# Optimization experiments

Measured on AMD Instinct MI355X. Metric: run time of the kernel, lower is better.

The kernel has to match this reference:

```python
import jax, jax.numpy as jnp
import numpy as np

N, S, E, H = 2, 2048, 1024, 16
D = E // H  # head dim = 64


def setup_inputs() -> dict:
    key = jax.random.key(0)
    ks = jax.random.split(key, 9)
    queries = jax.random.normal(ks[0], (N, S, E), dtype=jnp.float32)
    keys = jax.random.normal(ks[1], (N, S, E), dtype=jnp.float32)
    values = jax.random.normal(ks[2], (N, S, E), dtype=jnp.float32)
    mask = jax.random.randint(ks[3], (N, H, S, S), 0, 2, dtype=jnp.int32)
    # torch nn.Linear weights: shape (out_features, in_features), y = x @ W.T
    sc = 1.0 / np.sqrt(E)
    Wq = jax.random.uniform(ks[4], (E, E), jnp.float32, -sc, sc)
    Wk = jax.random.uniform(ks[5], (E, E), jnp.float32, -sc, sc)
    Wv = jax.random.uniform(ks[6], (E, E), jnp.float32, -sc, sc)
    Wo = jax.random.uniform(ks[7], (E, E), jnp.float32, -sc, sc)
    bo = jax.random.uniform(ks[8], (E,), jnp.float32, -sc, sc)
    return {"queries": queries, "keys": keys, "values": values, "mask": mask,
            "Wq": Wq, "Wk": Wk, "Wv": Wv, "Wo": Wo, "bo": bo}


def reference(queries, keys, values, mask, Wq, Wk, Wv, Wo, bo):
    n, d_q, _ = queries.shape
    d_k = keys.shape[1]
    q = (queries @ Wq.T).reshape(n, d_q, H, D)
    k = (keys @ Wk.T).reshape(n, d_k, H, D)
    v = (values @ Wv.T).reshape(n, d_k, H, D)
    energy = jnp.einsum('nqhd,nkhd->nhqk', q, k)
    energy = jnp.where(mask == 0, jnp.float32(-1e20), energy)
    # NOTE: module scales by sqrt of KEY SEQUENCE LENGTH, not head dim
    attn = jax.nn.softmax(energy / (d_k ** 0.5), axis=3)
    out = jnp.einsum('nhql,nlhd->nqhd', attn, v).reshape(n, d_q, E)
    return out @ Wo.T + bo
```

## Files before the change

kernel.cpp:

```cpp
#include <hip/hip_runtime.h>
#include <hip/hip_bf16.h>

#define DEVI __device__ __forceinline__

typedef __bf16 bf16x8 __attribute__((ext_vector_type(8)));
typedef float f32x4 __attribute__((ext_vector_type(4)));
typedef unsigned short u16x4 __attribute__((ext_vector_type(4)));
typedef unsigned int u32x2 __attribute__((ext_vector_type(2)));
typedef unsigned long long ull;
typedef ull u64x2 __attribute__((ext_vector_type(2)));

constexpr int Nn = 2, Ss = 2048, Ee = 1024, Hh = 16;
constexpr int Ms = Nn * Ss;
constexpr float SCALE = 0.022097086912079608f;
constexpr int NCH = 524288;

constexpr size_t SZ_X   = (size_t)Ms * Ee;
constexpr size_t EEc    = (size_t)Ee * Ee;
constexpr size_t OFF_QB = 0;
constexpr size_t OFF_KB = SZ_X;
constexpr size_t OFF_VB = 2 * SZ_X;
constexpr size_t OFF_XQ = 3 * SZ_X;
constexpr size_t OFF_W  = 6 * SZ_X;
constexpr size_t OFF_PACK = 6 * SZ_X + 4 * EEc;
constexpr size_t OFF_ATTN = OFF_XQ;

DEVI unsigned short f2bf(float f) {
  unsigned int u = __builtin_bit_cast(unsigned int, f);
  u += 0x7fffu + ((u >> 16) & 1u);
  return (unsigned short)(u >> 16);
}

DEVI void async16(const void* g, void* l) {
  __builtin_amdgcn_global_load_lds(
      (const __attribute__((address_space(1))) void*)g,
      (__attribute__((address_space(3))) void*)l, 16, 0, 0);
}

DEVI f32x4 mfma_bf16(bf16x8 a, bf16x8 b, f32x4 c) {
  return __builtin_amdgcn_mfma_f32_16x16x32_bf16(a, b, c, 0, 0, 0);
}

DEVI unsigned cvt_pk_bf16(float lo, float hi) {
  unsigned r;
  asm("v_cvt_pk_bf16_f32 %0, %1, %2" : "=v"(r) : "v"(lo), "v"(hi));
  return r;
}

__global__ __launch_bounds__(256) void cvt_batch(
    const float* __restrict__ s0, const float* __restrict__ s1,
    const float* __restrict__ s2, const float* __restrict__ s3,
    unsigned short* __restrict__ dbase, size_t dstride, int n4)
{
  const float* s = (blockIdx.z == 0) ? s0 : (blockIdx.z == 1) ? s1
                 : (blockIdx.z == 2) ? s2 : s3;
  unsigned short* d = dbase + (size_t)blockIdx.z * dstride;
  const int i = blockIdx.x * 256 + threadIdx.x;
  if (i >= n4) return;
  const float4 v = reinterpret_cast<const float4*>(s)[i];
  u16x4 o = { f2bf(v.x), f2bf(v.y), f2bf(v.z), f2bf(v.w) };
  reinterpret_cast<u16x4*>(d)[i] = o;
}

__global__ __launch_bounds__(256) void qkv_pack(
    const unsigned short* __restrict__ Xq,
    const unsigned short* __restrict__ W,
    unsigned short* __restrict__ QKout,
    unsigned short* __restrict__ Vtout,
    const int* __restrict__ mask,
    ull* __restrict__ P64)
{
  constexpr int K = 1024;
  __shared__ unsigned short As[128 * 32];
  __shared__ unsigned short Bs[128 * 32];
  const int b = blockIdx.x;

  const unsigned short *A, *B;
  unsigned short* C;
  int ldC, m0, n0;
  if (b < 512) {
    const int z = b >> 8, by = (b >> 3) & 31, bx = b & 7;
    A = Xq + (size_t)z * SZ_X;  B = W + (size_t)z * EEc;
    C = QKout + (size_t)z * SZ_X;  ldC = Ee;  m0 = by * 128;  n0 = bx * 128;
  } else {
    const int v = b - 512, bx = v & 31, by = v >> 5;
    A = W + 2 * EEc;  B = Xq + 2 * SZ_X;
    C = Vtout;  ldC = Ms;  m0 = by * 128;  n0 = bx * 128;
  }

  const int tid = threadIdx.x;
  const int lane = tid & 63, w = tid >> 6;
  const int lr = lane & 15, lg = lane >> 4;
  const int wr = (w >> 1) * 64, wc = (w & 1) * 64;

  const f32x4 zero = {0.f, 0.f, 0.f, 0.f};
  f32x4 acc[4][4];
  for (int a = 0; a < 4; ++a)
    for (int c = 0; c < 4; ++c) acc[a][c] = zero;

  const int cblock = b * 768;

  for (int s = 0; s < 32; ++s) {
    const int k0 = s * 32;
#pragma unroll
    for (int ii = 0; ii < 2; ++ii) {
      const int i = 2 * w + ii;
      const int boff = i * 1024 + lane * 16;
      const int row = boff >> 6;
      const int colb = boff & 63;
      const char* ga = (const char*)A + ((size_t)(m0 + row) * K + k0) * 2 + colb;
      const char* gb = (const char*)B + ((size_t)(n0 + row) * K + k0) * 2 + colb;
      async16(ga, (char*)As + i * 1024);
      async16(gb, (char*)Bs + i * 1024);
    }

    const int cbase = cblock + s * 24 + w * 6;
    int pm[6][4];
#pragma unroll
    for (int i = 0; i < 6; ++i) {
      const int ch = cbase + i;
      if (ch < NCH) {
        const int* mp = mask + (size_t)ch * 256 + lane;
        pm[i][0] = __builtin_nontemporal_load(mp);
        pm[i][1] = __builtin_nontemporal_load(mp + 64);
        pm[i][2] = __builtin_nontemporal_load(mp + 128);
        pm[i][3] = __builtin_nontemporal_load(mp + 192);
      }
    }

    __syncthreads();

    bf16x8 aF[4], bF[4];
#pragma unroll
    for (int rb = 0; rb < 4; ++rb)
      aF[rb] = *(const bf16x8*)(As + (wr + rb * 16 + lr) * 32 + lg * 8);
#pragma unroll
    for (int cb = 0; cb < 4; ++cb)
      bF[cb] = *(const bf16x8*)(Bs + (wc + cb * 16 + lr) * 32 + lg * 8);
#pragma unroll
    for (int rb = 0; rb < 4; ++rb)
#pragma unroll
      for (int cb = 0; cb < 4; ++cb)
        acc[rb][cb] = mfma_bf16(aF[rb], bF[cb], acc[rb][cb]);

#pragma unroll
    for (int i = 0; i < 6; ++i) {
      const int ch = cbase + i;
      if (ch < NCH) {
        const ull b0 = __ballot(pm[i][0] != 0);
        const ull b1 = __ballot(pm[i][1] != 0);
        const ull b2 = __ballot(pm[i][2] != 0);
        const ull b3 = __ballot(pm[i][3] != 0);
        if (lane < 2) {
          u64x2 v;
          v[0] = lane == 0 ? b0 : b2;
          v[1] = lane == 0 ? b1 : b3;
          *(u64x2*)(P64 + (size_t)ch * 4 + lane * 2) = v;
        }
      }
    }

    __syncthreads();
  }

#pragma unroll
  for (int rb = 0; rb < 4; ++rb)
#pragma unroll
    for (int cb = 0; cb < 4; ++cb)
#pragma unroll
      for (int j = 0; j < 4; ++j) {
        const int row = m0 + wr + rb * 16 + lg * 4 + j;
        const int col = n0 + wc + cb * 16 + lr;
        C[(size_t)row * ldC + col] = f2bf(acc[rb][cb][j]);
      }
}

__global__ __launch_bounds__(256) void attn_kernel(
    const unsigned short* __restrict__ Qb,
    const unsigned short* __restrict__ Kb,
    const unsigned short* __restrict__ Vtb,
    const ull* __restrict__ P64,
    unsigned short* __restrict__ Ob)
{
  __shared__ unsigned short Kl0[64 * 64], Kl1[64 * 64];
  __shared__ unsigned short Vl0[64 * 64], Vl1[64 * 64];
  __shared__ unsigned short Pw[4 * 32 * 72];

  const int tid = threadIdx.x;
  const int lane = tid & 63, w = tid >> 6;
  const int lr = lane & 15, lg = lane >> 4;

  const int lid = blockIdx.x;
  const int xcd = lid & 7, slot = lid >> 3;
  const int g = xcd + 8 * (slot >> 4);
  const int n = g >> 4, h = g & 15;
  const int q0 = (slot & 15) * 128;

  bf16x8 aQ[2][2];
#pragma unroll
  for (int qb = 0; qb < 2; ++qb) {
    const unsigned short* qp =
        Qb + ((size_t)(n * Ss + q0 + w * 32 + qb * 16 + lr)) * Ee + h * 64 + lg * 8;
    aQ[qb][0] = *(const bf16x8*)(qp);
    aQ[qb][1] = *(const bf16x8*)(qp + 32);
  }

  const int sig0 = (w * 2) * 64 + lane;
  const int row0 = sig0 >> 3;
  const int c0 = (sig0 & 7) ^ (row0 & 7);
  const int row1 = row0 + 8;
  const int c1 = (sig0 & 7) ^ (row1 & 7);
  const int ldsb0 = (w * 2 + 0) * 1024;
  const int ldsb1 = (w * 2 + 1) * 1024;

  const unsigned short* kp0 = Kb + ((size_t)(n * Ss + row0) * Ee + h * 64 + c0 * 8);
  const unsigned short* kp1 = Kb + ((size_t)(n * Ss + row1) * Ee + h * 64 + c1 * 8);
  const unsigned short* vp0 = Vtb + ((size_t)(h * 64 + row0) * Ms + n * Ss + c0 * 8);
  const unsigned short* vp1 = Vtb + ((size_t)(h * 64 + row1) * Ms + n * Ss + c1 * 8);

  const ull* bmr0 = P64 + ((size_t)(n * Hh + h) * Ss + q0 + w * 32 + lr) * 32;
  const ull* bmr1 = bmr0 + 16 * 32;

  int koff[4][2];
#pragma unroll
  for (int cb = 0; cb < 4; ++cb) {
    const int row = cb * 16 + lr;
    koff[cb][0] = row * 128 + ((lg ^ (row & 7)) * 16);
    koff[cb][1] = row * 128 + (((4 + lg) ^ (row & 7)) * 16);
  }
  char* const PwW = (char*)Pw + w * (32 * 144);
  int pwo[2], pro[2];
#pragma unroll
  for (int qb = 0; qb < 2; ++qb) {
    pwo[qb] = (qb * 16 + lr) * 144 + lg * 8;
    pro[qb] = (qb * 16 + lr) * 144 + lg * 16;
  }

  const f32x4 zero = {0.f, 0.f, 0.f, 0.f};
  f32x4 oacc[2][4];
#pragma unroll
  for (int qb = 0; qb < 2; ++qb)
#pragma unroll
    for (int db = 0; db < 4; ++db) oacc[qb][db] = zero;
  float rs[2] = {0.f, 0.f};

  async16(kp0, (char*)Kl0 + ldsb0);
  async16(kp1, (char*)Kl0 + ldsb1);
  async16(vp0, (char*)Vl0 + ldsb0);
  async16(vp1, (char*)Vl0 + ldsb1);
  kp0 += (size_t)64 * Ee; kp1 += (size_t)64 * Ee; vp0 += 64; vp1 += 64;

  u64x2 bmA[2], bmB[2];
  bmA[0] = *(const u64x2*)(bmr0);      bmA[1] = *(const u64x2*)(bmr1);
  bmB[0] = *(const u64x2*)(bmr0 + 2);  bmB[1] = *(const u64x2*)(bmr1 + 2);

  auto tile = [&](const unsigned short* KC, const unsigned short* VC,
                  unsigned short* KN, unsigned short* VN,
                  const u64x2* BM, int tp, u64x2* BMN, int tn, bool do_stage) {
    asm volatile("s_waitcnt vmcnt(0)" ::: "memory");
    __builtin_amdgcn_s_barrier();

    if (do_stage) {
      async16(kp0, (char*)KN + ldsb0);
      async16(kp1, (char*)KN + ldsb1);
      async16(vp0, (char*)VN + ldsb0);
      async16(vp1, (char*)VN + ldsb1);
      kp0 += (size_t)64 * Ee; kp1 += (size_t)64 * Ee; vp0 += 64; vp1 += 64;
    }
    if (BMN) {
      BMN[0] = *(const u64x2*)(bmr0 + tn);
      BMN[1] = *(const u64x2*)(bmr1 + tn);
    }

#pragma unroll
    for (int cb = 0; cb < 4; ++cb) {
      const bf16x8 kF0 = *(const bf16x8*)((const char*)KC + koff[cb][0]);
      const bf16x8 kF1 = *(const bf16x8*)((const char*)KC + koff[cb][1]);
#pragma unroll
      for (int qb = 0; qb < 2; ++qb) {
        f32x4 a = mfma_bf16(kF0, aQ[qb][0], zero);
        a = mfma_bf16(kF1, aQ[qb][1], a);
        const unsigned nib =
            (unsigned)(BM[qb][tp] >> (cb * 16 + lg * 4)) & 0xFu;
        float p[4];
#pragma unroll
        for (int j = 0; j < 4; ++j)
          p[j] = (nib & (1u << j)) ? __expf(a[j] * SCALE) : 0.f;
        rs[qb] += (p[0] + p[1]) + (p[2] + p[3]);
        u32x2 pd = { cvt_pk_bf16(p[0], p[1]), cvt_pk_bf16(p[2], p[3]) };
        *(u32x2*)(PwW + pwo[qb] + cb * 32) = pd;
      }
    }

    bf16x8 aP[2][2];
#pragma unroll
    for (int qb = 0; qb < 2; ++qb) {
      aP[qb][0] = *(const bf16x8*)(PwW + pro[qb]);
      aP[qb][1] = *(const bf16x8*)(PwW + pro[qb] + 64);
    }
#pragma unroll
    for (int db = 0; db < 4; ++db) {
#pragma unroll
      for (int kc = 0; kc < 2; ++kc) {
        const bf16x8 bV = *(const bf16x8*)((const char*)VC + koff[db][kc]);
#pragma unroll
        for (int qb = 0; qb < 2; ++qb)
          oacc[qb][db] = mfma_bf16(aP[qb][kc], bV, oacc[qb][db]);
      }
    }
  };

  for (int t4 = 0; t4 < 8; ++t4) {
    const int t = t4 * 4;
    tile(Kl0, Vl0, Kl1, Vl1, bmA, 0, bmB, t + 2, true);
    tile(Kl1, Vl1, Kl0, Vl0, bmA, 1, nullptr, 0, true);
    tile(Kl0, Vl0, Kl1, Vl1, bmB, 0,
         (t4 != 7) ? bmA : nullptr, t + 4, true);
    tile(Kl1, Vl1, Kl0, Vl0, bmB, 1, nullptr, 0, t4 != 7);
  }

  float inv[2][4];
#pragma unroll
  for (int qb = 0; qb < 2; ++qb) {
    float r = rs[qb];
    r += __shfl_xor(r, 16, 64);
    r += __shfl_xor(r, 32, 64);
#pragma unroll
    for (int j = 0; j < 4; ++j)
      inv[qb][j] = 1.0f / __shfl(r, lg * 4 + j, 64);
  }
#pragma unroll
  for (int qb = 0; qb < 2; ++qb)
#pragma unroll
    for (int db = 0; db < 4; ++db)
#pragma unroll
      for (int j = 0; j < 4; ++j) {
        const int qr = q0 + w * 32 + qb * 16 + lg * 4 + j;
        Ob[((size_t)(n * Ss + qr)) * Ee + h * 64 + db * 16 + lr] =
            f2bf(oacc[qb][db][j] * inv[qb][j]);
      }
}

__global__ __launch_bounds__(256) void out_proj(
    const unsigned short* __restrict__ A,
    const unsigned short* __restrict__ B,
    float* __restrict__ Cf, const float* __restrict__ bias)
{
  __shared__ unsigned short As[128 * 32];
  __shared__ unsigned short Bs[128 * 32];
  constexpr int K = 1024;
  const int tid = threadIdx.x;
  const int lane = tid & 63, w = tid >> 6;
  const int lr = lane & 15, lg = lane >> 4;
  const int m0 = blockIdx.y * 128, n0 = blockIdx.x * 128;
  const int wr = (w >> 1) * 64, wc = (w & 1) * 64;

  const f32x4 zero = {0.f, 0.f, 0.f, 0.f};
  f32x4 acc[4][4];
  for (int a = 0; a < 4; ++a)
    for (int b = 0; b < 4; ++b) acc[a][b] = zero;

  for (int k0 = 0; k0 < K; k0 += 32) {
#pragma unroll
    for (int ii = 0; ii < 2; ++ii) {
      const int i = 2 * w + ii;
      const int boff = i * 1024 + lane * 16;
      const int row = boff >> 6;
      const int colb = boff & 63;
      const char* ga = (const char*)A + ((size_t)(m0 + row) * K + k0) * 2 + colb;
      const char* gb = (const char*)B + ((size_t)(n0 + row) * K + k0) * 2 + colb;
      async16(ga, (char*)As + i * 1024);
      async16(gb, (char*)Bs + i * 1024);
    }
    __syncthreads();

    bf16x8 aF[4], bF[4];
#pragma unroll
    for (int rb = 0; rb < 4; ++rb)
      aF[rb] = *(const bf16x8*)(As + (wr + rb * 16 + lr) * 32 + lg * 8);
#pragma unroll
    for (int cb = 0; cb < 4; ++cb)
      bF[cb] = *(const bf16x8*)(Bs + (wc + cb * 16 + lr) * 32 + lg * 8);
#pragma unroll
    for (int rb = 0; rb < 4; ++rb)
#pragma unroll
      for (int cb = 0; cb < 4; ++cb)
        acc[rb][cb] = mfma_bf16(aF[rb], bF[cb], acc[rb][cb]);
    __syncthreads();
  }

#pragma unroll
  for (int rb = 0; rb < 4; ++rb)
#pragma unroll
    for (int cb = 0; cb < 4; ++cb)
#pragma unroll
      for (int j = 0; j < 4; ++j) {
        const int row = m0 + wr + rb * 16 + lg * 4 + j;
        const int col = n0 + wc + cb * 16 + lr;
        Cf[(size_t)row * Ee + col] = acc[rb][cb][j] + bias[col];
      }
}

extern "C" void kernel_launch(void* const* d_in, const int* in_sizes, int n_in,
                              void* d_out, int out_size, void* d_ws, size_t ws_size,
                              hipStream_t stream) {
  const float* qin = (const float*)d_in[0];
  const float* kin = (const float*)d_in[1];
  const float* vin = (const float*)d_in[2];
  const int*   msk = (const int*)d_in[3];
  const float* Wq  = (const float*)d_in[4];
  const float* Wk  = (const float*)d_in[5];
  const float* Wv  = (const float*)d_in[6];
  const float* Wo  = (const float*)d_in[7];
  const float* bo  = (const float*)d_in[8];
  unsigned short* ws = (unsigned short*)d_ws;
  ull* P64 = (ull*)(ws + OFF_PACK);

  cvt_batch<<<dim3((unsigned)(SZ_X / 4 / 256), 1, 3), 256, 0, stream>>>(
      qin, kin, vin, nullptr, ws + OFF_XQ, SZ_X, (int)(SZ_X / 4));
  cvt_batch<<<dim3((unsigned)(EEc / 4 / 256), 1, 4), 256, 0, stream>>>(
      Wq, Wk, Wv, Wo, ws + OFF_W, EEc, (int)(EEc / 4));

  qkv_pack<<<dim3(768), 256, 0, stream>>>(
      ws + OFF_XQ, ws + OFF_W, ws + OFF_QB, ws + OFF_VB, msk, P64);

  attn_kernel<<<dim3(512), 256, 0, stream>>>(
      ws + OFF_QB, ws + OFF_KB, ws + OFF_VB, P64, ws + OFF_ATTN);

  out_proj<<<dim3(8, 32), 256, 0, stream>>>(
      ws + OFF_ATTN, ws + OFF_W + 3 * EEc, (float*)d_out, bo);
}
```

Measured before the change: 246.8 us.

## Double-buffer qkv_pack shared tiles and prefetch mask chunks one stage ahead

```diff
diff --git a/kernel.cpp b/kernel.cpp
--- a/kernel.cpp
+++ b/kernel.cpp
@@ -62,7 +62,7 @@
   reinterpret_cast<u16x4*>(d)[i] = o;
 }
 
-__global__ __launch_bounds__(256) void qkv_pack(
+__global__ __launch_bounds__(256, 3) void qkv_pack(
     const unsigned short* __restrict__ Xq,
     const unsigned short* __restrict__ W,
     unsigned short* __restrict__ QKout,
@@ -71,8 +71,8 @@
     ull* __restrict__ P64)
 {
   constexpr int K = 1024;
-  __shared__ unsigned short As[128 * 32];
-  __shared__ unsigned short Bs[128 * 32];
+  __shared__ unsigned short As0[128 * 32], As1[128 * 32];
+  __shared__ unsigned short Bs0[128 * 32], Bs1[128 * 32];
   const int b = blockIdx.x;
 
   const unsigned short *A, *B;
@@ -93,29 +93,32 @@
   const int lr = lane & 15, lg = lane >> 4;
   const int wr = (w >> 1) * 64, wc = (w & 1) * 64;
 
+  const int i0 = 2 * w, i1 = 2 * w + 1;
+  const int boff0 = i0 * 1024 + lane * 16, boff1 = i1 * 1024 + lane * 16;
+  const int srow0 = boff0 >> 6, scol0 = boff0 & 63;
+  const int srow1 = boff1 >> 6, scol1 = boff1 & 63;
+
   const f32x4 zero = {0.f, 0.f, 0.f, 0.f};
   f32x4 acc[4][4];
   for (int a = 0; a < 4; ++a)
     for (int c = 0; c < 4; ++c) acc[a][c] = zero;
 
   const int cblock = b * 768;
-
-  for (int s = 0; s < 32; ++s) {
+  int pm[6][4];
+
+  auto stage = [&](int s, unsigned short* An, unsigned short* Bn) {
     const int k0 = s * 32;
-#pragma unroll
-    for (int ii = 0; ii < 2; ++ii) {
-      const int i = 2 * w + ii;
-      const int boff = i * 1024 + lane * 16;
-      const int row = boff >> 6;
-      const int colb = boff & 63;
-      const char* ga = (const char*)A + ((size_t)(m0 + row) * K + k0) * 2 + colb;
-      const char* gb = (const char*)B + ((size_t)(n0 + row) * K + k0) * 2 + colb;
-      async16(ga, (char*)As + i * 1024);
-      async16(gb, (char*)Bs + i * 1024);
-    }
-
+    async16((const char*)A + ((size_t)(m0 + srow0) * K + k0) * 2 + scol0,
+            (char*)An + i0 * 1024);
+    async16((const char*)B + ((size_t)(n0 + srow0) * K + k0) * 2 + scol0,
+            (char*)Bn + i0 * 1024);
+    async16((const char*)A + ((size_t)(m0 + srow1) * K + k0) * 2 + scol1,
+            (char*)An + i1 * 1024);
+    async16((const char*)B + ((size_t)(n0 + srow1) * K + k0) * 2 + scol1,
+            (char*)Bn + i1 * 1024);
+  };
+  auto mload = [&](int s) {
     const int cbase = cblock + s * 24 + w * 6;
-    int pm[6][4];
 #pragma unroll
     for (int i = 0; i < 6; ++i) {
       const int ch = cbase + i;
@@ -127,40 +130,56 @@
         pm[i][3] = __builtin_nontemporal_load(mp + 192);
       }
     }
-
-    __syncthreads();
+  };
+
+  stage(0, As0, Bs0);
+  mload(0);
+
+  auto step = [&](int s, unsigned short* Ac, unsigned short* Bc,
+                  unsigned short* An, unsigned short* Bn) {
+    asm volatile("s_waitcnt vmcnt(0)" ::: "memory");
+    __builtin_amdgcn_s_barrier();
+
+    if (s + 1 < 32) stage(s + 1, An, Bn);
+
+    {
+      const int cbase = cblock + s * 24 + w * 6;
+#pragma unroll
+      for (int i = 0; i < 6; ++i) {
+        const int ch = cbase + i;
+        if (ch < NCH) {
+          const ull b0 = __ballot(pm[i][0] != 0);
+          const ull b1 = __ballot(pm[i][1] != 0);
+          const ull b2 = __ballot(pm[i][2] != 0);
+          const ull b3 = __ballot(pm[i][3] != 0);
+          if (lane < 2) {
+            u64x2 v;
+            v[0] = lane == 0 ? b0 : b2;
+            v[1] = lane == 0 ? b1 : b3;
+            *(u64x2*)(P64 + (size_t)ch * 4 + lane * 2) = v;
+          }
+        }
+      }
+    }
+    if (s + 1 < 32) mload(s + 1);
 
     bf16x8 aF[4], bF[4];
 #pragma unroll
     for (int rb = 0; rb < 4; ++rb)
-      aF[rb] = *(const bf16x8*)(As + (wr + rb * 16 + lr) * 32 + lg * 8);
+      aF[rb] = *(const bf16x8*)(Ac + (wr + rb * 16 + lr) * 32 + lg * 8);
 #pragma unroll
     for (int cb = 0; cb < 4; ++cb)
-      bF[cb] = *(const bf16x8*)(Bs + (wc + cb * 16 + lr) * 32 + lg * 8);
+      bF[cb] = *(const bf16x8*)(Bc + (wc + cb * 16 + lr) * 32 + lg * 8);
 #pragma unroll
     for (int rb = 0; rb < 4; ++rb)
 #pragma unroll
       for (int cb = 0; cb < 4; ++cb)
         acc[rb][cb] = mfma_bf16(aF[rb], bF[cb], acc[rb][cb]);
-
-#pragma unroll
-    for (int i = 0; i < 6; ++i) {
-      const int ch = cbase + i;
-      if (ch < NCH) {
-        const ull b0 = __ballot(pm[i][0] != 0);
-        const ull b1 = __ballot(pm[i][1] != 0);
-        const ull b2 = __ballot(pm[i][2] != 0);
-        const ull b3 = __ballot(pm[i][3] != 0);
-        if (lane < 2) {
-          u64x2 v;
-          v[0] = lane == 0 ? b0 : b2;
-          v[1] = lane == 0 ? b1 : b3;
-          *(u64x2*)(P64 + (size_t)ch * 4 + lane * 2) = v;
-        }
-      }
-    }
-
-    __syncthreads();
+  };
+
+  for (int s2 = 0; s2 < 16; ++s2) {
+    step(2 * s2,     As0, Bs0, As1, Bs1);
+    step(2 * s2 + 1, As1, Bs1, As0, Bs0);
   }
 
 #pragma unroll
```

After: 253.4 us. +2.7%, slower.
